# Optimization experiments

Measured on AMD Instinct MI355X. Metric: run time of the kernel, lower is better.

## Reference

```python
import jax, jax.numpy as jnp
import numpy as np

N_STATES = 21


def setup_inputs() -> dict:
    key = jax.random.key(0)
    ks = jax.random.split(key, 12)
    N_pulses, B = 128, 8192
    u = lambda k, shape, lo, hi: jax.random.uniform(k, shape, jnp.float32, lo, hi)
    return {
        "flip_angles": u(ks[0], (N_pulses,), 0.0, jnp.pi / 2),  # rad
        "phases": u(ks[1], (N_pulses,), 0.0, 2 * jnp.pi),
        "T1f": u(ks[2], (B,), 800.0, 1500.0),   # ms
        "T2f": u(ks[3], (B,), 50.0, 100.0),
        "T1b": u(ks[4], (B,), 200.0, 400.0),
        "T2b": u(ks[5], (B,), 8.0, 20.0),
        "kf": u(ks[6], (B,), 1.0, 5.0),
        "kb": u(ks[7], (B,), 1.0, 5.0),
        "B0": jax.random.normal(ks[8], (B,), jnp.float32) * 20.0,  # Hz
        "B1": u(ks[9], (B,), 0.8, 1.2),
        "wf": u(ks[10], (B,), 0.85, 0.95),
        "wb": u(ks[11], (B,), 0.05, 0.15),
        "TR": 10,
        "TE": 5,
    }


def _simulate(flip_angles, phases, T1f, T2f, T1b, T2b, kf, kb, B0, B1, wf, wb, TR):
    B = T1f.shape[0]
    col = lambda v: v.astype(jnp.float32)[:, None]  # (B,1) for broadcast over states
    T1f, T2f, T1b, T2b = col(T1f), col(T2f), col(T1b), col(T2b)
    kf, kb, B0, B1, wf, wb = col(kf), col(kb), col(B0), col(B1), col(wf), col(wb)
    TR = jnp.float32(TR)
    E1f, E2f = jnp.exp(-TR / T1f), jnp.exp(-TR / T2f)
    E1b, E2b = jnp.exp(-TR / T1b), jnp.exp(-TR / T2b)
    phi = 2.0 * jnp.pi * B0 * TR / 1000.0
    b0_p = jnp.exp(1j * phi).astype(jnp.complex64)   # (B,1)
    b0_m = jnp.conj(b0_p)
    dt = TR / 1000.0

    czeros = jnp.zeros((B, N_STATES), jnp.complex64)
    Zf0 = jnp.zeros((B, N_STATES), jnp.float32).at[:, 0].set(wf[:, 0])
    Zb0 = jnp.zeros((B, N_STATES), jnp.float32).at[:, 0].set(wb[:, 0])
    carry0 = (czeros, czeros, Zf0, czeros, czeros, Zb0)

    def shift(Fp, Fm, Z):
        Fp = jnp.roll(Fp, 1, axis=1).at[:, 0].set(0)
        Fm = jnp.roll(Fm, -1, axis=1).at[:, -1].set(0)
        Z = jnp.roll(Z, 1, axis=1).at[:, 0].set(0)
        return Fp, Fm, Z

    def step(carry, fa_ph):
        Fpf, Fmf, Zf, Fpb, Fmb, Zb = carry
        fa, ph = fa_ph
        # --- relax + exchange ---
        Fpf, Fmf = Fpf * E2f, Fmf * E2f
        Fpb, Fmb = Fpb * E2b, Fmb * E2b
        dZf = (-kf * Zf + kb * Zb) * dt
        dZb = (-kb * Zb + kf * Zf) * dt
        Zf_t1 = (Zf * E1f).at[:, 0].add((1.0 - E1f[:, 0]) * wf[:, 0])
        Zb_t1 = (Zb * E1b).at[:, 0].add((1.0 - E1b[:, 0]) * wb[:, 0])
        Zf, Zb = Zf_t1 + dZf, Zb_t1 + dZb
        # --- B0 precession (both pools) ---
        Fpf, Fmf = Fpf * b0_p, Fmf * b0_m
        Fpb, Fmb = Fpb * b0_p, Fmb * b0_m
        # --- RF pulse (free pool only, as in the torch code) ---
        alpha = fa * B1  # (B,1)
        ca, sa = jnp.cos(alpha / 2), jnp.sin(alpha / 2)
        eib = jnp.exp(1j * ph).astype(jnp.complex64)
        emib = jnp.conj(eib)
        Fpf_n = ca**2 * Fpf + sa**2 * jnp.conj(Fmf) * eib**2 + 1j * ca * sa * (Zf * eib)
        Fmf_n = sa**2 * jnp.conj(Fpf) * emib**2 + ca**2 * Fmf - 1j * ca * sa * (Zf * emib)
        Zf_n = (-1j * sa * ca * (Fpf * emib - Fmf * eib) + (ca**2 - sa**2) * Zf).real
        Fpf, Fmf, Zf = Fpf_n, Fmf_n, Zf_n
        # --- EPG shift (both pools) ---
        Fpf, Fmf, Zf = shift(Fpf, Fmf, Zf)
        Fpb, Fmb, Zb = shift(Fpb, Fmb, Zb)
        carry = (Fpf, Fmf, Zf, Fpb, Fmb, Zb)
        # real-valued packed state: (B, n_states, 10)
        out = jnp.stack([Fpf.real, Fpf.imag, Fmf.real, Fmf.imag, Zf,
                         Fpb.real, Fpb.imag, Fmb.real, Fmb.imag, Zb], axis=-1)
        return carry, out

    xs = (flip_angles.astype(jnp.float32), phases.astype(jnp.float32))
    _, states = jax.lax.scan(step, carry0, xs)
    return states  # (N_pulses, B, n_states, 10)


def reference(flip_angles, phases, T1f, T2f, T1b, T2b, kf, kb, B0, B1, wf, wb, TR, TE):
    # TE is accepted (matches the torch signature) but unused by the simulation.
    return _simulate(flip_angles, phases, T1f, T2f, T1b, T2b, kf, kb, B0, B1, wf, wb, TR)
```

## Files before the change

kernel.cpp:

```cpp
#include <hip/hip_runtime.h>
#include <math.h>

#define NSTATES 21
#define NPULSES 128
#define BATCH   8192
#define BPB     12

typedef float v4f __attribute__((ext_vector_type(4)));

__global__ __launch_bounds__(256) void epg_mt_kernel(
    const float* __restrict__ fa_arr,
    const float* __restrict__ ph_arr,
    const float* __restrict__ T1f, const float* __restrict__ T2f,
    const float* __restrict__ T1b, const float* __restrict__ T2b,
    const float* __restrict__ kfp, const float* __restrict__ kbp,
    const float* __restrict__ B0p, const float* __restrict__ B1p,
    const float* __restrict__ wfp, const float* __restrict__ wbp,
    const int*   __restrict__ TRp,
    float* __restrict__ out)
{
    __shared__ float lds[2][BPB * NSTATES * 10];

    const int tid  = threadIdx.x;
    const int lane = tid & 63;
    const int g    = lane / 21;
    const int s    = lane - g * 21;
    const int lb   = (tid >> 6) * 3 + g;
    const int b0   = blockIdx.x * BPB;
    const int b    = b0 + lb;
    const bool valid = (g < 3) && (b < BATCH);
    const int bc   = valid ? b : 0;

    for (int i = tid; i < 2 * BPB * NSTATES * 10; i += 256)
        ((float*)lds)[i] = 0.f;

    const float tr  = (float)TRp[0];
    const float dt  = tr * 0.001f;
    const float E1f = expf(-tr / T1f[bc]);
    const float E2f = expf(-tr / T2f[bc]);
    const float E1b = expf(-tr / T1b[bc]);
    const float kfdt = kfp[bc] * dt;
    const float kbdt = kbp[bc] * dt;
    const float phi  = 6.28318530717958647692f * B0p[bc] * dt;
    const float b0c  = cosf(phi), b0s = sinf(phi);
    const float wfv  = wfp[bc], wbv = wbp[bc];
    const float add0f = (s == 0) ? (1.0f - E1f) * wfv : 0.0f;
    const float add0b = (s == 0) ? (1.0f - E1b) * wbv : 0.0f;
    const float b1   = B1p[bc];

    float Fpr = 0.f, Fpi = 0.f, Fmr = 0.f, Fmi = 0.f;
    float Zf = (s == 0) ? wfv : 0.f;
    float Zb = (s == 0) ? wbv : 0.f;

    const int nb = (BATCH - b0 < BPB) ? (BATCH - b0) : BPB;
    const int n4 = (nb * NSTATES * 10) >> 2;
    const size_t pstride = (size_t)BATCH * NSTATES * 10;
    float* outb = out + (size_t)b0 * (NSTATES * 10);

    auto step = [&](float fa, float ph) {
        Fpr *= E2f; Fpi *= E2f; Fmr *= E2f; Fmi *= E2f;
        const float dZf = kbdt * Zb - kfdt * Zf;
        const float dZb = kfdt * Zf - kbdt * Zb;
        const float nZf1 = fmaf(Zf, E1f, add0f) + dZf;
        const float nZb1 = fmaf(Zb, E1b, add0b) + dZb;
        Zf = nZf1; Zb = nZb1;
        {
            const float r  = Fpr * b0c - Fpi * b0s;
            const float i_ = Fpr * b0s + Fpi * b0c;
            const float r2 = Fmr * b0c + Fmi * b0s;
            const float i2 = Fmi * b0c - Fmr * b0s;
            Fpr = r; Fpi = i_; Fmr = r2; Fmi = i2;
        }
        const float half = 0.5f * fa * b1;
        const float ca = __cosf(half), sa = __sinf(half);
        const float cph = __cosf(ph), sph = __sinf(ph);
        const float ca2 = ca * ca, sa2 = sa * sa, casa = ca * sa;
        const float cd  = ca2 - sa2;
        const float e2c = cph * cph - sph * sph;
        const float e2s = 2.f * cph * sph;
        const float t1r = Fmr * e2c + Fmi * e2s;
        const float t1i = Fmr * e2s - Fmi * e2c;
        const float t2r = Fpr * e2c - Fpi * e2s;
        const float t2i = -(Fpr * e2s) - Fpi * e2c;
        const float zc = Zf * cph, zs = Zf * sph;
        const float nFpr = ca2 * Fpr + sa2 * t1r - casa * zs;
        const float nFpi = ca2 * Fpi + sa2 * t1i + casa * zc;
        const float nFmr = sa2 * t2r + ca2 * Fmr - casa * zs;
        const float nFmi = sa2 * t2i + ca2 * Fmi - casa * zc;
        const float nZf = casa * ((Fpi * cph - Fpr * sph) - (Fmi * cph + Fmr * sph)) + cd * Zf;
        Fpr = nFpr; Fpi = nFpi; Fmr = nFmr; Fmi = nFmi; Zf = nZf;
        const float sFpr = __shfl_up(Fpr, 1);
        const float sFpi = __shfl_up(Fpi, 1);
        const float sZf  = __shfl_up(Zf, 1);
        const float sZb  = __shfl_up(Zb, 1);
        const float sFmr = __shfl_down(Fmr, 1);
        const float sFmi = __shfl_down(Fmi, 1);
        const bool s0 = (s == 0), sE = (s == NSTATES - 1);
        Fpr = s0 ? 0.f : sFpr;
        Fpi = s0 ? 0.f : sFpi;
        Zf  = s0 ? 0.f : sZf;
        Zb  = s0 ? 0.f : sZb;
        Fmr = sE ? 0.f : sFmr;
        Fmi = sE ? 0.f : sFmi;
    };

    asm volatile("s_waitcnt lgkmcnt(0)" ::: "memory");
    __builtin_amdgcn_s_barrier();

    step(fa_arr[0], ph_arr[0]);

    for (int p = 0; p < NPULSES; ++p) {
        if (valid) {
            float* dst = lds[p & 1] + lb * (NSTATES * 10) + s * 10;
            ((float2*)dst)[0] = make_float2(Fpr, Fpi);
            ((float2*)dst)[1] = make_float2(Fmr, Fmi);
            dst[4] = Zf;
            dst[9] = Zb;
        }
        asm volatile("s_waitcnt lgkmcnt(0)" ::: "memory");
        __builtin_amdgcn_s_barrier();

        if (p + 1 < NPULSES)
            step(fa_arr[p + 1], ph_arr[p + 1]);

        const v4f* Ls = (const v4f*)(lds[p & 1]);
        v4f* og = (v4f*)(outb + (size_t)p * pstride);
        for (int i = tid; i < n4; i += 256) {
            v4f tmp = Ls[i];
            __builtin_nontemporal_store(tmp, &og[i]);
        }
    }
}

extern "C" void kernel_launch(void* const* d_in, const int* in_sizes, int n_in,
                              void* d_out, int out_size, void* d_ws, size_t ws_size,
                              hipStream_t stream) {
    const float* fa  = (const float*)d_in[0];
    const float* ph  = (const float*)d_in[1];
    const float* T1f = (const float*)d_in[2];
    const float* T2f = (const float*)d_in[3];
    const float* T1b = (const float*)d_in[4];
    const float* T2b = (const float*)d_in[5];
    const float* kf  = (const float*)d_in[6];
    const float* kb  = (const float*)d_in[7];
    const float* B0  = (const float*)d_in[8];
    const float* B1  = (const float*)d_in[9];
    const float* wf  = (const float*)d_in[10];
    const float* wb  = (const float*)d_in[11];
    const int*   TR  = (const int*)d_in[12];
    float* out = (float*)d_out;

    const int blocks = (BATCH + BPB - 1) / BPB;
    epg_mt_kernel<<<blocks, 256, 0, stream>>>(fa, ph, T1f, T2f, T1b, T2b,
                                              kf, kb, B0, B1, wf, wb, TR, out);
}
```

Before: 219.9 us.

## Warp-specialize compute and store waves with chunked LDS double-buffering

```diff
diff --git a/kernel.cpp b/kernel.cpp
--- a/kernel.cpp
+++ b/kernel.cpp
@@ -5,10 +5,15 @@
 #define NPULSES 128
 #define BATCH   8192
 #define BPB     12
+#define CHUNK   4
+#define NCHUNK  (NPULSES / CHUNK)
+#define RECF    (NSTATES * 10)
+#define PFLOATS (BPB * RECF)
+#define N4FULL  (PFLOATS / 4)
 
 typedef float v4f __attribute__((ext_vector_type(4)));
 
-__global__ __launch_bounds__(256) void epg_mt_kernel(
+__global__ __launch_bounds__(512) void epg_mt_kernel(
     const float* __restrict__ fa_arr,
     const float* __restrict__ ph_arr,
     const float* __restrict__ T1f, const float* __restrict__ T2f,
@@ -19,115 +24,141 @@
     const int*   __restrict__ TRp,
     float* __restrict__ out)
 {
-    __shared__ float lds[2][BPB * NSTATES * 10];
+    __shared__ __attribute__((aligned(16))) float lds[2][CHUNK][PFLOATS];
 
-    const int tid  = threadIdx.x;
-    const int lane = tid & 63;
-    const int g    = lane / 21;
-    const int s    = lane - g * 21;
-    const int lb   = (tid >> 6) * 3 + g;
-    const int b0   = blockIdx.x * BPB;
-    const int b    = b0 + lb;
-    const bool valid = (g < 3) && (b < BATCH);
-    const int bc   = valid ? b : 0;
+    const int tid = threadIdx.x;
+    const int wv  = tid >> 6;
 
-    for (int i = tid; i < 2 * BPB * NSTATES * 10; i += 256)
+    for (int i = tid; i < 2 * CHUNK * PFLOATS; i += 512)
         ((float*)lds)[i] = 0.f;
 
-    const float tr  = (float)TRp[0];
-    const float dt  = tr * 0.001f;
-    const float E1f = expf(-tr / T1f[bc]);
-    const float E2f = expf(-tr / T2f[bc]);
-    const float E1b = expf(-tr / T1b[bc]);
-    const float kfdt = kfp[bc] * dt;
-    const float kbdt = kbp[bc] * dt;
-    const float phi  = 6.28318530717958647692f * B0p[bc] * dt;
-    const float b0c  = cosf(phi), b0s = sinf(phi);
-    const float wfv  = wfp[bc], wbv = wbp[bc];
-    const float add0f = (s == 0) ? (1.0f - E1f) * wfv : 0.0f;
-    const float add0b = (s == 0) ? (1.0f - E1b) * wbv : 0.0f;
-    const float b1   = B1p[bc];
+    const int b0 = blockIdx.x * BPB;
+    const int nb = (BATCH - b0 < BPB) ? (BATCH - b0) : BPB;
+    const int n4 = (nb * RECF) >> 2;
+    const size_t pstride4 = ((size_t)BATCH * RECF) >> 2;
+    v4f* outb4 = ((v4f*)out) + (size_t)blockIdx.x * N4FULL;
 
-    float Fpr = 0.f, Fpi = 0.f, Fmr = 0.f, Fmi = 0.f;
-    float Zf = (s == 0) ? wfv : 0.f;
-    float Zb = (s == 0) ? wbv : 0.f;
+    if (wv < 4) {
+        const int lane = tid & 63;
+        const int g    = lane / 21;
+        const int s    = lane - g * 21;
+        const int lb   = wv * 3 + g;
+        const bool valid = (g < 3) && (lb < nb);
+        const int bc   = valid ? (b0 + lb) : 0;
 
-    const int nb = (BATCH - b0 < BPB) ? (BATCH - b0) : BPB;
-    const int n4 = (nb * NSTATES * 10) >> 2;
-    const size_t pstride = (size_t)BATCH * NSTATES * 10;
-    float* outb = out + (size_t)b0 * (NSTATES * 10);
+        const float tr  = (float)TRp[0];
+        const float dt  = tr * 0.001f;
+        const float E1f = expf(-tr / T1f[bc]);
+        const float E2f = expf(-tr / T2f[bc]);
+        const float E1b = expf(-tr / T1b[bc]);
+        const float kfdt = kfp[bc] * dt;
+        const float kbdt = kbp[bc] * dt;
+        const float phi  = 6.28318530717958647692f * B0p[bc] * dt;
+        const float b0c  = cosf(phi), b0s = sinf(phi);
+        const float wfv  = wfp[bc], wbv = wbp[bc];
+        const float add0f = (s == 0) ? (1.0f - E1f) * wfv : 0.0f;
+        const float add0b = (s == 0) ? (1.0f - E1b) * wbv : 0.0f;
+        const float b1   = B1p[bc];
 
-    auto step = [&](float fa, float ph) {
-        Fpr *= E2f; Fpi *= E2f; Fmr *= E2f; Fmi *= E2f;
-        const float dZf = kbdt * Zb - kfdt * Zf;
-        const float dZb = kfdt * Zf - kbdt * Zb;
-        const float nZf1 = fmaf(Zf, E1f, add0f) + dZf;
-        const float nZb1 = fmaf(Zb, E1b, add0b) + dZb;
-        Zf = nZf1; Zb = nZb1;
-        {
-            const float r  = Fpr * b0c - Fpi * b0s;
-            const float i_ = Fpr * b0s + Fpi * b0c;
-            const float r2 = Fmr * b0c + Fmi * b0s;
-            const float i2 = Fmi * b0c - Fmr * b0s;
-            Fpr = r; Fpi = i_; Fmr = r2; Fmi = i2;
-        }
-        const float half = 0.5f * fa * b1;
-        const float ca = __cosf(half), sa = __sinf(half);
-        const float cph = __cosf(ph), sph = __sinf(ph);
-        const float ca2 = ca * ca, sa2 = sa * sa, casa = ca * sa;
-        const float cd  = ca2 - sa2;
-        const float e2c = cph * cph - sph * sph;
-        const float e2s = 2.f * cph * sph;
-        const float t1r = Fmr * e2c + Fmi * e2s;
-        const float t1i = Fmr * e2s - Fmi * e2c;
-        const float t2r = Fpr * e2c - Fpi * e2s;
-        const float t2i = -(Fpr * e2s) - Fpi * e2c;
-        const float zc = Zf * cph, zs = Zf * sph;
-        const float nFpr = ca2 * Fpr + sa2 * t1r - casa * zs;
-        const float nFpi = ca2 * Fpi + sa2 * t1i + casa * zc;
-        const float nFmr = sa2 * t2r + ca2 * Fmr - casa * zs;
-        const float nFmi = sa2 * t2i + ca2 * Fmi - casa * zc;
-        const float nZf = casa * ((Fpi * cph - Fpr * sph) - (Fmi * cph + Fmr * sph)) + cd * Zf;
-        Fpr = nFpr; Fpi = nFpi; Fmr = nFmr; Fmi = nFmi; Zf = nZf;
-        const float sFpr = __shfl_up(Fpr, 1);
-        const float sFpi = __shfl_up(Fpi, 1);
-        const float sZf  = __shfl_up(Zf, 1);
-        const float sZb  = __shfl_up(Zb, 1);
-        const float sFmr = __shfl_down(Fmr, 1);
-        const float sFmi = __shfl_down(Fmi, 1);
-        const bool s0 = (s == 0), sE = (s == NSTATES - 1);
-        Fpr = s0 ? 0.f : sFpr;
-        Fpi = s0 ? 0.f : sFpi;
-        Zf  = s0 ? 0.f : sZf;
-        Zb  = s0 ? 0.f : sZb;
-        Fmr = sE ? 0.f : sFmr;
-        Fmi = sE ? 0.f : sFmi;
-    };
+        float Fpr = 0.f, Fpi = 0.f, Fmr = 0.f, Fmi = 0.f;
+        float Zf = (s == 0) ? wfv : 0.f;
+        float Zb = (s == 0) ? wbv : 0.f;
 
-    asm volatile("s_waitcnt lgkmcnt(0)" ::: "memory");
-    __builtin_amdgcn_s_barrier();
+        auto step = [&](float fa, float ph) {
+            Fpr *= E2f; Fpi *= E2f; Fmr *= E2f; Fmi *= E2f;
+            const float dZf = kbdt * Zb - kfdt * Zf;
+            const float dZb = kfdt * Zf - kbdt * Zb;
+            const float nZf1 = fmaf(Zf, E1f, add0f) + dZf;
+            const float nZb1 = fmaf(Zb, E1b, add0b) + dZb;
+            Zf = nZf1; Zb = nZb1;
+            {
+                const float r  = Fpr * b0c - Fpi * b0s;
+                const float i_ = Fpr * b0s + Fpi * b0c;
+                const float r2 = Fmr * b0c + Fmi * b0s;
+                const float i2 = Fmi * b0c - Fmr * b0s;
+                Fpr = r; Fpi = i_; Fmr = r2; Fmi = i2;
+            }
+            const float half = 0.5f * fa * b1;
+            const float ca = __cosf(half), sa = __sinf(half);
+            const float cph = __cosf(ph), sph = __sinf(ph);
+            const float ca2 = ca * ca, sa2 = sa * sa, casa = ca * sa;
+            const float cd  = ca2 - sa2;
+            const float e2c = cph * cph - sph * sph;
+            const float e2s = 2.f * cph * sph;
+            const float t1r = Fmr * e2c + Fmi * e2s;
+            const float t1i = Fmr * e2s - Fmi * e2c;
+            const float t2r = Fpr * e2c - Fpi * e2s;
+            const float t2i = -(Fpr * e2s) - Fpi * e2c;
+            const float zc = Zf * cph, zs = Zf * sph;
+            const float nFpr = ca2 * Fpr + sa2 * t1r - casa * zs;
+            const float nFpi = ca2 * Fpi + sa2 * t1i + casa * zc;
+            const float nFmr = sa2 * t2r + ca2 * Fmr - casa * zs;
+            const float nFmi = sa2 * t2i + ca2 * Fmi - casa * zc;
+            const float nZf = casa * ((Fpi * cph - Fpr * sph) - (Fmi * cph + Fmr * sph)) + cd * Zf;
+            Fpr = nFpr; Fpi = nFpi; Fmr = nFmr; Fmi = nFmi; Zf = nZf;
+            const float sFpr = __shfl_up(Fpr, 1);
+            const float sFpi = __shfl_up(Fpi, 1);
+            const float sZf  = __shfl_up(Zf, 1);
+            const float sZb  = __shfl_up(Zb, 1);
+            const float sFmr = __shfl_down(Fmr, 1);
+            const float sFmi = __shfl_down(Fmi, 1);
+            const bool s0 = (s == 0), sE = (s == NSTATES - 1);
+            Fpr = s0 ? 0.f : sFpr;
+            Fpi = s0 ? 0.f : sFpi;
+            Zf  = s0 ? 0.f : sZf;
+            Zb  = s0 ? 0.f : sZb;
+            Fmr = sE ? 0.f : sFmr;
+            Fmi = sE ? 0.f : sFmi;
+        };
 
-    step(fa_arr[0], ph_arr[0]);
+        auto stage_chunk = [&](int c) {
+            #pragma unroll
+            for (int cp = 0; cp < CHUNK; ++cp) {
+                step(fa_arr[c * CHUNK + cp], ph_arr[c * CHUNK + cp]);
+                if (valid) {
+                    float* dst = &lds[c & 1][cp][lb * RECF + s * 10];
+                    ((float2*)dst)[0] = make_float2(Fpr, Fpi);
+                    ((float2*)dst)[1] = make_float2(Fmr, Fmi);
+                    dst[4] = Zf;
+                    dst[9] = Zb;
+                }
+            }
+        };
 
-    for (int p = 0; p < NPULSES; ++p) {
-        if (valid) {
-            float* dst = lds[p & 1] + lb * (NSTATES * 10) + s * 10;
-            ((float2*)dst)[0] = make_float2(Fpr, Fpi);
-            ((float2*)dst)[1] = make_float2(Fmr, Fmi);
-            dst[4] = Zf;
-            dst[9] = Zb;
-        }
+        stage_chunk(0);
         asm volatile("s_waitcnt lgkmcnt(0)" ::: "memory");
         __builtin_amdgcn_s_barrier();
 
-        if (p + 1 < NPULSES)
-            step(fa_arr[p + 1], ph_arr[p + 1]);
+        for (int c = 0; c < NCHUNK; ++c) {
+            if (c + 1 < NCHUNK)
+                stage_chunk(c + 1);
+            asm volatile("s_waitcnt lgkmcnt(0)" ::: "memory");
+            __builtin_amdgcn_s_barrier();
+        }
+    } else {
+        const int wtid = tid - 256;
 
-        const v4f* Ls = (const v4f*)(lds[p & 1]);
-        v4f* og = (v4f*)(outb + (size_t)p * pstride);
-        for (int i = tid; i < n4; i += 256) {
-            v4f tmp = Ls[i];
-            __builtin_nontemporal_store(tmp, &og[i]);
+        asm volatile("s_waitcnt lgkmcnt(0)" ::: "memory");
+        __builtin_amdgcn_s_barrier();
+
+        for (int c = 0; c < NCHUNK; ++c) {
+            const float* Lb = (const float*)lds[c & 1];
+            #pragma unroll
+            for (int cp = 0; cp < CHUNK; ++cp) {
+                const v4f* Ls = (const v4f*)(Lb + cp * PFLOATS);
+                v4f* og = outb4 + (size_t)(c * CHUNK + cp) * pstride4;
+                const int i0 = wtid, i1 = wtid + 256, i2 = wtid + 512;
+                v4f t0, t1, t2;
+                t0 = Ls[i0];
+                const bool v1 = (i1 < n4), v2 = (i2 < n4);
+                if (v1) t1 = Ls[i1];
+                if (v2) t2 = Ls[i2];
+                og[i0] = t0;
+                if (v1) og[i1] = t1;
+                if (v2) og[i2] = t2;
+            }
+            asm volatile("s_waitcnt lgkmcnt(0)" ::: "memory");
+            __builtin_amdgcn_s_barrier();
         }
     }
 }
@@ -151,6 +182,6 @@
     float* out = (float*)d_out;
 
     const int blocks = (BATCH + BPB - 1) / BPB;
-    epg_mt_kernel<<<blocks, 256, 0, stream>>>(fa, ph, T1f, T2f, T1b, T2b,
+    epg_mt_kernel<<<blocks, 512, 0, stream>>>(fa, ph, T1f, T2f, T1b, T2b,
                                               kf, kb, B0, B1, wf, wb, TR, out);
 }
```

New measurement: 207.1 us. -5.8%, faster.
